# Kernel optimization log

Hardware: AMD Instinct MI355X
Metric: run time of the kernel (lower is better)

## Reference

```python
import jax, jax.numpy as jnp
import numpy as np

NUM_HEADS = 12


def setup_inputs() -> dict:
    key = jax.random.key(0)
    ks = jax.random.split(key, 4)
    N, L, C = 32, 577, 768  # L = 24*24 patches + 1 cls token
    x = jax.random.normal(ks[0], (N, L, C), dtype=jnp.float32)
    w_qkv = jax.random.normal(ks[1], (3 * C, C), dtype=jnp.float32) * 0.02
    w_proj = jax.random.normal(ks[2], (C, C), dtype=jnp.float32) * 0.02
    b_proj = jnp.zeros((C,), dtype=jnp.float32)
    w_dwc = jax.random.normal(ks[3], (C, 1, 3, 3), dtype=jnp.float32) * 0.02
    b_dwc = jnp.zeros((C,), dtype=jnp.float32)
    return {"x": x, "w_qkv": w_qkv, "w_proj": w_proj, "b_proj": b_proj,
            "w_dwc": w_dwc, "b_dwc": b_dwc}


def reference(x, w_qkv, w_proj, b_proj, w_dwc, b_dwc):
    N, L, C = x.shape
    H = NUM_HEADS
    hd = C // H
    h = w = int(L ** 0.5)  # 24; h*w == L-1 (cls token excluded)

    # qkv transform: (N, L, 3C) -> (3, N, H, L, hd)
    qkv = (x @ w_qkv.T).reshape(N, L, 3, H, hd).transpose(2, 0, 3, 1, 4)
    q, k, v = qkv[0], qkv[1], qkv[2]

    # graph-candidate attention (default: scaled dot-product softmax)
    scale = hd ** -0.5
    scores = jnp.einsum('bhqd,bhkd->bhqk', q, k) * scale
    attn = jax.nn.softmax(scores, axis=-1)
    out = jnp.einsum('bhqk,bhkd->bhqd', attn, v)  # (N, H, L, hd)
    out = out.transpose(0, 2, 1, 3).reshape(N, L, C)

    # depthwise conv on v (patch tokens only), NCHW layout
    v_ = v[:, :, 1:, :].transpose(0, 2, 1, 3).reshape(N, h, w, C).transpose(0, 3, 1, 2)
    dwc = jax.lax.conv_general_dilated(
        v_, w_dwc, window_strides=(1, 1), padding=((1, 1), (1, 1)),
        dimension_numbers=('NCHW', 'OIHW', 'NCHW'), feature_group_count=C)
    dwc = dwc + b_dwc[None, :, None, None]
    dwc = dwc.transpose(0, 2, 3, 1).reshape(N, L - 1, C)

    out = out.at[:, 1:, :].add(dwc)
    out = out @ w_proj.T + b_proj
    return out
```

## Files before the change

### kernel.cpp

```cpp
#include <hip/hip_runtime.h>

typedef short bf16x8 __attribute__((ext_vector_type(8)));
typedef float f32x4 __attribute__((ext_vector_type(4)));
typedef unsigned short u16;

#define NB 32
#define LSEQ 577
#define CD 768
#define NH 12
#define HD 64
#define MROWS (NB * LSEQ)
#define LPAD 584

#define GLD16(g, l)                                                    \
  __builtin_amdgcn_global_load_lds(                                    \
      (const __attribute__((address_space(1))) void*)(g),              \
      (__attribute__((address_space(3))) void*)(l), 16, 0, 0)

__device__ __forceinline__ u16 f2bf(float f) {
  union { float f; unsigned u; } v; v.f = f;
  unsigned u = v.u + 0x7fffu + ((v.u >> 16) & 1u);
  return (u16)(u >> 16);
}
__device__ __forceinline__ float bf2f(u16 s) {
  union { unsigned u; float f; } v; v.u = ((unsigned)s) << 16;
  return v.f;
}

__global__ __launch_bounds__(256) void cvt_bf16(
    const float* __restrict__ src, u16* __restrict__ dst, int n4) {
  int i = blockIdx.x * 256 + threadIdx.x;
  if (i < n4) {
    float4 v = reinterpret_cast<const float4*>(src)[i];
    ushort4 o;
    o.x = f2bf(v.x); o.y = f2bf(v.y); o.z = f2bf(v.z); o.w = f2bf(v.w);
    reinterpret_cast<ushort4*>(dst)[i] = o;
  }
}

__global__ __launch_bounds__(512, 2) void qkv_gemm(
    const u16* __restrict__ xb, const u16* __restrict__ wqb,
    u16* __restrict__ qb, u16* __restrict__ kb, u16* __restrict__ vtb) {
  __shared__ __align__(16) u16 As[3][256 * 32];
  __shared__ __align__(16) u16 Bs[3][256 * 32];
  const int m0 = blockIdx.x * 256;
  const int n0 = blockIdx.y * 256;
  const int t = threadIdx.x;
  const int lane = t & 63, wid = t >> 6;
  const int wm = wid >> 2, wn = wid & 3;
  const int g = lane >> 4, cl = lane & 15;

  const int r16 = lane >> 2;
  const int scol = (lane & 3) * 8;
  const int ra0 = wid * 16 + r16;
  const int ra1 = 128 + wid * 16 + r16;
  int gm0 = m0 + ra0; gm0 = gm0 < MROWS ? gm0 : MROWS - 1;
  int gm1 = m0 + ra1; gm1 = gm1 < MROWS ? gm1 : MROWS - 1;
  const u16* ax0 = xb + (size_t)gm0 * CD + scol;
  const u16* ax1 = xb + (size_t)gm1 * CD + scol;
  const u16* bx0 = wqb + (size_t)(n0 + ra0) * CD + scol;
  const u16* bx1 = wqb + (size_t)(n0 + ra1) * CD + scol;

  const f32x4 fz = {0.f, 0.f, 0.f, 0.f};
  f32x4 acc[8][4];
#pragma unroll
  for (int i = 0; i < 8; ++i)
#pragma unroll
    for (int j = 0; j < 4; ++j) acc[i][j] = fz;

#define QSTAGE(b, kt)                                  \
  do {                                                 \
    int kc = (kt) * 32;                                \
    GLD16(ax0 + kc, &As[b][wid * 512]);                \
    GLD16(ax1 + kc, &As[b][(wid + 8) * 512]);          \
    GLD16(bx0 + kc, &Bs[b][wid * 512]);                \
    GLD16(bx1 + kc, &Bs[b][(wid + 8) * 512]);          \
  } while (0)

  QSTAGE(0, 0);
  QSTAGE(1, 1);
  for (int kt = 0; kt < 24; ++kt) {
    const int cb = kt % 3;
    if (kt < 23) asm volatile("s_waitcnt vmcnt(4)" ::: "memory");
    else         asm volatile("s_waitcnt vmcnt(0)" ::: "memory");
    __builtin_amdgcn_s_barrier();
    if (kt < 22) QSTAGE((kt + 2) % 3, kt + 2);
    bf16x8 af[8], bfv[4];
#pragma unroll
    for (int mt = 0; mt < 8; ++mt)
      af[mt] = *reinterpret_cast<const bf16x8*>(&As[cb][(wm * 128 + mt * 16 + cl) * 32 + g * 8]);
#pragma unroll
    for (int nt = 0; nt < 4; ++nt)
      bfv[nt] = *reinterpret_cast<const bf16x8*>(&Bs[cb][(wn * 64 + nt * 16 + cl) * 32 + g * 8]);
    __builtin_amdgcn_s_setprio(1);
#pragma unroll
    for (int mt = 0; mt < 8; ++mt)
#pragma unroll
      for (int nt = 0; nt < 4; ++nt)
        acc[mt][nt] = __builtin_amdgcn_mfma_f32_16x16x32_bf16(af[mt], bfv[nt], acc[mt][nt], 0, 0, 0);
    __builtin_amdgcn_s_setprio(0);
  }
#undef QSTAGE

  const int which = n0 / CD;
  const int rem0 = n0 % CD;
#pragma unroll
  for (int mt = 0; mt < 8; ++mt) {
#pragma unroll
    for (int nt = 0; nt < 4; ++nt) {
      int rem = rem0 + wn * 64 + nt * 16 + cl;
      int hh = rem >> 6, d = rem & 63;
#pragma unroll
      for (int r = 0; r < 4; ++r) {
        int m = m0 + wm * 128 + mt * 16 + g * 4 + r;
        if (m < MROWS) {
          int nb = m / LSEQ, l = m - nb * LSEQ;
          if (which == 0)
            qb[(((size_t)nb * NH + hh) * LSEQ + l) * HD + d] = f2bf(acc[mt][nt][r] * 0.125f);
          else if (which == 1)
            kb[(((size_t)nb * NH + hh) * LSEQ + l) * HD + d] = f2bf(acc[mt][nt][r]);
          else
            vtb[(((size_t)nb * NH + hh) * HD + d) * LPAD + l] = f2bf(acc[mt][nt][r]);
        }
      }
    }
  }
}

__global__ __launch_bounds__(512) void attn_fwd(
    const u16* __restrict__ q, const u16* __restrict__ k,
    const u16* __restrict__ vt, u16* __restrict__ y) {
  __shared__ __align__(16) u16 Ks[64 * 72];
  __shared__ __align__(16) u16 Vts[64 * 72];
  __shared__ __align__(16) u16 Ps[8][16 * 72];

  const int qtile = blockIdx.x;
  const int h = blockIdx.y;
  const int nb = blockIdx.z;
  const int t = threadIdx.x;
  const int lane = t & 63, wid = t >> 6;
  const int g = lane >> 4, cl = lane & 15;

  const size_t hoff = ((size_t)nb * NH + h) * LSEQ * HD;
  const u16* qh = q + hoff;
  const u16* kh = k + hoff;
  const u16* vth = vt + ((size_t)nb * NH + h) * HD * LPAD;

  const int qbase = qtile * 128;
  const int qrow = qbase + wid * 16 + cl;
  const int qrc = qrow < LSEQ ? qrow : LSEQ - 1;
  bf16x8 qf0 = *reinterpret_cast<const bf16x8*>(qh + (size_t)qrc * HD + g * 8);
  bf16x8 qf1 = *reinterpret_cast<const bf16x8*>(qh + (size_t)qrc * HD + 32 + g * 8);

  const f32x4 fz = {0.f, 0.f, 0.f, 0.f};
  float mrow = -3.0e38f, lrow = 0.f;
  f32x4 oaccT[4];
#pragma unroll
  for (int dt = 0; dt < 4; ++dt) oaccT[dt] = fz;

  for (int kv = 0; kv < LSEQ; kv += 64) {
    {
      int row = t >> 3, c8 = (t & 7) << 3;
      int grow = kv + row;
      uint4 kd = {0, 0, 0, 0};
      if (grow < LSEQ) kd = *reinterpret_cast<const uint4*>(kh + (size_t)grow * HD + c8);
      *reinterpret_cast<uint4*>(&Ks[row * 72 + c8]) = kd;
      uint4 vd = *reinterpret_cast<const uint4*>(vth + (size_t)row * LPAD + kv + c8);
      *reinterpret_cast<uint4*>(&Vts[row * 72 + c8]) = vd;
    }
    __syncthreads();

    f32x4 sT[4];
#pragma unroll
    for (int nt = 0; nt < 4; ++nt) {
      bf16x8 a0 = *reinterpret_cast<const bf16x8*>(&Ks[(nt * 16 + cl) * 72 + g * 8]);
      bf16x8 a1 = *reinterpret_cast<const bf16x8*>(&Ks[(nt * 16 + cl) * 72 + 32 + g * 8]);
      f32x4 s = fz;
      s = __builtin_amdgcn_mfma_f32_16x16x32_bf16(a0, qf0, s, 0, 0, 0);
      s = __builtin_amdgcn_mfma_f32_16x16x32_bf16(a1, qf1, s, 0, 0, 0);
      sT[nt] = s;
    }

#pragma unroll
    for (int nt = 0; nt < 4; ++nt)
#pragma unroll
      for (int r = 0; r < 4; ++r)
        if (kv + nt * 16 + g * 4 + r >= LSEQ) sT[nt][r] = -3.0e38f;

    float pm = -3.0e38f;
#pragma unroll
    for (int nt = 0; nt < 4; ++nt)
#pragma unroll
      for (int r = 0; r < 4; ++r) pm = fmaxf(pm, sT[nt][r]);
    pm = fmaxf(pm, __shfl_xor(pm, 16));
    pm = fmaxf(pm, __shfl_xor(pm, 32));

    float nm = fmaxf(mrow, pm);
    float alpha = __expf(mrow - nm);
    mrow = nm;
    float ps = 0.f;
#pragma unroll
    for (int nt = 0; nt < 4; ++nt)
#pragma unroll
      for (int r = 0; r < 4; ++r) {
        float p = __expf(sT[nt][r] - nm);
        sT[nt][r] = p;
        ps += p;
      }
    ps += __shfl_xor(ps, 16);
    ps += __shfl_xor(ps, 32);
    lrow = lrow * alpha + ps;
#pragma unroll
    for (int dt = 0; dt < 4; ++dt) oaccT[dt] *= alpha;

#pragma unroll
    for (int nt = 0; nt < 4; ++nt) {
      ushort4 p4;
      p4.x = f2bf(sT[nt][0]); p4.y = f2bf(sT[nt][1]);
      p4.z = f2bf(sT[nt][2]); p4.w = f2bf(sT[nt][3]);
      *reinterpret_cast<ushort4*>(&Ps[wid][cl * 72 + nt * 16 + g * 4]) = p4;
    }
    __syncthreads();

#pragma unroll
    for (int kc = 0; kc < 2; ++kc) {
      bf16x8 pa = *reinterpret_cast<const bf16x8*>(&Ps[wid][cl * 72 + kc * 32 + g * 8]);
#pragma unroll
      for (int dt = 0; dt < 4; ++dt) {
        bf16x8 va = *reinterpret_cast<const bf16x8*>(&Vts[(dt * 16 + cl) * 72 + kc * 32 + g * 8]);
        oaccT[dt] = __builtin_amdgcn_mfma_f32_16x16x32_bf16(va, pa, oaccT[dt], 0, 0, 0);
      }
    }
    __syncthreads();
  }

  if (qrow < LSEQ) {
    float inv = 1.f / lrow;
#pragma unroll
    for (int dt = 0; dt < 4; ++dt) {
      ushort4 o4;
      o4.x = f2bf(oaccT[dt][0] * inv); o4.y = f2bf(oaccT[dt][1] * inv);
      o4.z = f2bf(oaccT[dt][2] * inv); o4.w = f2bf(oaccT[dt][3] * inv);
      *reinterpret_cast<ushort4*>(
          &y[((size_t)nb * LSEQ + qrow) * CD + h * HD + dt * 16 + g * 4]) = o4;
    }
  }
}

__global__ __launch_bounds__(256) void dwc_add(
    const u16* __restrict__ vt, const float* __restrict__ wd,
    const float* __restrict__ bd, u16* __restrict__ y) {
  __shared__ u16 V[32 * 588];
  const int d0 = blockIdx.x * 32;
  const int h = blockIdx.y;
  const int nb = blockIdx.z;
  const int t = threadIdx.x;
  const u16* vrow = vt + (((size_t)nb * NH + h) * HD + d0) * LPAD;

  for (int c = t; c < 32 * 73; c += 256) {
    int row = c / 73;
    int k0 = (c - row * 73) * 8;
    uint4 vv = *reinterpret_cast<const uint4*>(vrow + (size_t)row * LPAD + k0);
    const u16* vp = (const u16*)&vv;
    *reinterpret_cast<ushort4*>(&V[row * 588 + k0]) = *(const ushort4*)vp;
    *reinterpret_cast<ushort4*>(&V[row * 588 + k0 + 4]) = *(const ushort4*)(vp + 4);
  }
  __syncthreads();

  const int d = t & 31;
  const int c = h * HD + d0 + d;
  float w9[9];
#pragma unroll
  for (int j = 0; j < 9; ++j) w9[j] = wd[c * 9 + j];
  const float bias = bd[c];
  const u16* Vd = &V[d * 588];

  for (int it = 0; it < 72; ++it) {
    int li = (t >> 5) + it * 8;
    int py = li / 24, px = li - py * 24;
    float acc = bias;
#pragma unroll
    for (int ky = 0; ky < 3; ++ky) {
      int yy = py + ky - 1;
      if (yy < 0 || yy >= 24) continue;
      int base = 1 + yy * 24;
#pragma unroll
      for (int kx = 0; kx < 3; ++kx) {
        int xx = px + kx - 1;
        if (xx < 0 || xx >= 24) continue;
        acc += w9[ky * 3 + kx] * bf2f(Vd[base + xx]);
      }
    }
    size_t yi = ((size_t)nb * LSEQ + 1 + li) * CD + c;
    y[yi] = f2bf(bf2f(y[yi]) + acc);
  }
}

__global__ __launch_bounds__(256) void proj_gemm(
    const u16* __restrict__ yb, const u16* __restrict__ wpb,
    const float* __restrict__ bias, float* __restrict__ out) {
  __shared__ __align__(16) u16 As[2][128 * 32];
  __shared__ __align__(16) u16 Bs[2][128 * 32];
  const int m0 = blockIdx.x * 128;
  const int n0 = blockIdx.y * 128;
  const int t = threadIdx.x;
  const int lane = t & 63, wid = t >> 6;
  const int wm = wid >> 1, wn = wid & 1;
  const int g = lane >> 4, cl = lane & 15;

  const int srow = wid * 32 + (lane >> 2);
  const int scol = (lane & 3) * 8;
  int ga0 = m0 + srow;      ga0 = ga0 < MROWS ? ga0 : MROWS - 1;
  int ga1 = m0 + srow + 16; ga1 = ga1 < MROWS ? ga1 : MROWS - 1;
  const u16* asrc0 = yb + (size_t)ga0 * CD + scol;
  const u16* asrc1 = yb + (size_t)ga1 * CD + scol;
  const u16* bsrc0 = wpb + (size_t)(n0 + srow) * CD + scol;
  const u16* bsrc1 = wpb + (size_t)(n0 + srow + 16) * CD + scol;

  const f32x4 fz = {0.f, 0.f, 0.f, 0.f};
  f32x4 acc[4][4];
#pragma unroll
  for (int i = 0; i < 4; ++i)
#pragma unroll
    for (int j = 0; j < 4; ++j) acc[i][j] = fz;

#define PSTAGE(b, kt)                                   \
  do {                                                  \
    int kc = (kt) * 32;                                 \
    GLD16(asrc0 + kc, &As[b][wid * 1024]);              \
    GLD16(asrc1 + kc, &As[b][wid * 1024 + 512]);        \
    GLD16(bsrc0 + kc, &Bs[b][wid * 1024]);              \
    GLD16(bsrc1 + kc, &Bs[b][wid * 1024 + 512]);        \
  } while (0)

  PSTAGE(0, 0);
  __syncthreads();
  int cur = 0;
  for (int kt = 0; kt < 24; ++kt) {
    if (kt < 23) PSTAGE(cur ^ 1, kt + 1);
    bf16x8 af[4], bfv[4];
#pragma unroll
    for (int mt = 0; mt < 4; ++mt)
      af[mt] = *reinterpret_cast<const bf16x8*>(&As[cur][(wm * 64 + mt * 16 + cl) * 32 + g * 8]);
#pragma unroll
    for (int nt = 0; nt < 4; ++nt)
      bfv[nt] = *reinterpret_cast<const bf16x8*>(&Bs[cur][(wn * 64 + nt * 16 + cl) * 32 + g * 8]);
    __builtin_amdgcn_s_setprio(1);
#pragma unroll
    for (int mt = 0; mt < 4; ++mt)
#pragma unroll
      for (int nt = 0; nt < 4; ++nt)
        acc[mt][nt] = __builtin_amdgcn_mfma_f32_16x16x32_bf16(af[mt], bfv[nt], acc[mt][nt], 0, 0, 0);
    __builtin_amdgcn_s_setprio(0);
    __syncthreads();
    cur ^= 1;
  }
#undef PSTAGE

#pragma unroll
  for (int nt = 0; nt < 4; ++nt) {
    int n = n0 + wn * 64 + nt * 16 + cl;
    float bn = bias[n];
#pragma unroll
    for (int mt = 0; mt < 4; ++mt)
#pragma unroll
      for (int r = 0; r < 4; ++r) {
        int m = m0 + wm * 64 + mt * 16 + g * 4 + r;
        if (m < MROWS) out[(size_t)m * CD + n] = acc[mt][nt][r] + bn;
      }
  }
}

extern "C" void kernel_launch(void* const* d_in, const int* in_sizes, int n_in,
                              void* d_out, int out_size, void* d_ws, size_t ws_size,
                              hipStream_t stream) {
  const float* x = (const float*)d_in[0];
  const float* w_qkv = (const float*)d_in[1];
  const float* w_proj = (const float*)d_in[2];
  const float* b_proj = (const float*)d_in[3];
  const float* w_dwc = (const float*)d_in[4];
  const float* b_dwc = (const float*)d_in[5];
  float* out = (float*)d_out;

  const size_t SEG = (size_t)NB * NH * LSEQ * HD;
  const size_t SEGT = (size_t)NB * NH * HD * LPAD;
  const size_t YN = (size_t)MROWS * CD;
  u16* yb = (u16*)d_ws;
  u16* xb = yb;
  u16* qb = yb + YN;
  u16* kb = qb + SEG;
  u16* vtb = kb + SEG;
  u16* wqb = vtb + SEGT;
  u16* wpb = wqb + (size_t)3 * CD * CD;

  cvt_bf16<<<dim3((int)(YN / 4 / 256)), 256, 0, stream>>>(x, xb, (int)(YN / 4));
  cvt_bf16<<<dim3(3 * CD * CD / 4 / 256), 256, 0, stream>>>(w_qkv, wqb, 3 * CD * CD / 4);
  cvt_bf16<<<dim3(CD * CD / 4 / 256), 256, 0, stream>>>(w_proj, wpb, CD * CD / 4);
  qkv_gemm<<<dim3(73, 9), 512, 0, stream>>>(xb, wqb, qb, kb, vtb);
  attn_fwd<<<dim3(5, 12, 32), 512, 0, stream>>>(qb, kb, vtb, yb);
  dwc_add<<<dim3(2, 12, 32), 256, 0, stream>>>(vtb, w_dwc, b_dwc, yb);
  proj_gemm<<<dim3(145, 6), 256, 0, stream>>>(yb, wpb, b_proj, out);
}
```

Baseline: 394.4 us.

## Remap GEMM blocks per XCD, double-buffer attention K/V, inline-asm LDS reads

Both GEMMs now use a 1D grid whose block ids are remapped so each XCD processes a contiguous range of output tiles, aiming for better L2 reuse of A/B panels. The QKV GEMM loads its fragments from LDS with explicit ds_read_b128 asm, followed by a full lgkmcnt wait and a sched barrier. The attention kernel double-buffers K/V tiles in LDS: the next tile is prefetched into registers during compute and stored afterwards, which removes one syncthreads per iteration and adds setprio around the MFMAs. The costs are more LDS use in attention and fixed schedules that the compiler can no longer reorder.

```diff
diff --git a/kernel.cpp b/kernel.cpp
--- a/kernel.cpp
+++ b/kernel.cpp
@@ -3,6 +3,7 @@
 typedef short bf16x8 __attribute__((ext_vector_type(8)));
 typedef float f32x4 __attribute__((ext_vector_type(4)));
 typedef unsigned short u16;
+typedef __attribute__((address_space(3))) const u16* lds_cptr;
 
 #define NB 32
 #define LSEQ 577
@@ -16,6 +17,10 @@
   __builtin_amdgcn_global_load_lds(                                    \
       (const __attribute__((address_space(1))) void*)(g),              \
       (__attribute__((address_space(3))) void*)(l), 16, 0, 0)
+
+#define DSR(dst, base, ofs)                                            \
+  asm volatile("ds_read_b128 %0, %1 offset:" #ofs                      \
+               : "=v"(dst) : "v"((lds_cptr)(base)))
 
 __device__ __forceinline__ u16 f2bf(float f) {
   union { float f; unsigned u; } v; v.f = f;
@@ -43,8 +48,11 @@
     u16* __restrict__ qb, u16* __restrict__ kb, u16* __restrict__ vtb) {
   __shared__ __align__(16) u16 As[3][256 * 32];
   __shared__ __align__(16) u16 Bs[3][256 * 32];
-  const int m0 = blockIdx.x * 256;
-  const int n0 = blockIdx.y * 256;
+  const int id = blockIdx.x;
+  const int xcd = id & 7, pos = id >> 3;
+  const int wg = (xcd == 0 ? pos : 83 + (xcd - 1) * 82 + pos);
+  const int m0 = (wg / 9) * 256;
+  const int n0 = (wg % 9) * 256;
   const int t = threadIdx.x;
   const int lane = t & 63, wid = t >> 6;
   const int wm = wid >> 2, wn = wid & 3;
@@ -81,17 +89,21 @@
   QSTAGE(1, 1);
   for (int kt = 0; kt < 24; ++kt) {
     const int cb = kt % 3;
-    if (kt < 23) asm volatile("s_waitcnt vmcnt(4)" ::: "memory");
-    else         asm volatile("s_waitcnt vmcnt(0)" ::: "memory");
+    if (kt < 23) asm volatile("s_waitcnt vmcnt(4)");
+    else         asm volatile("s_waitcnt vmcnt(0)");
     __builtin_amdgcn_s_barrier();
     if (kt < 22) QSTAGE((kt + 2) % 3, kt + 2);
+    const u16* pa = &As[cb][(wm * 128 + cl) * 32 + g * 8];
+    const u16* pb = &Bs[cb][(wn * 64 + cl) * 32 + g * 8];
     bf16x8 af[8], bfv[4];
-#pragma unroll
-    for (int mt = 0; mt < 8; ++mt)
-      af[mt] = *reinterpret_cast<const bf16x8*>(&As[cb][(wm * 128 + mt * 16 + cl) * 32 + g * 8]);
-#pragma unroll
-    for (int nt = 0; nt < 4; ++nt)
-      bfv[nt] = *reinterpret_cast<const bf16x8*>(&Bs[cb][(wn * 64 + nt * 16 + cl) * 32 + g * 8]);
+    DSR(af[0], pa, 0);    DSR(af[1], pa, 1024);
+    DSR(af[2], pa, 2048); DSR(af[3], pa, 3072);
+    DSR(af[4], pa, 4096); DSR(af[5], pa, 5120);
+    DSR(af[6], pa, 6144); DSR(af[7], pa, 7168);
+    DSR(bfv[0], pb, 0);    DSR(bfv[1], pb, 1024);
+    DSR(bfv[2], pb, 2048); DSR(bfv[3], pb, 3072);
+    asm volatile("s_waitcnt lgkmcnt(0)");
+    __builtin_amdgcn_sched_barrier(0);
     __builtin_amdgcn_s_setprio(1);
 #pragma unroll
     for (int mt = 0; mt < 8; ++mt)
@@ -130,15 +142,15 @@
 __global__ __launch_bounds__(512) void attn_fwd(
     const u16* __restrict__ q, const u16* __restrict__ k,
     const u16* __restrict__ vt, u16* __restrict__ y) {
-  __shared__ __align__(16) u16 Ks[64 * 72];
-  __shared__ __align__(16) u16 Vts[64 * 72];
+  __shared__ __align__(16) u16 Ks[2][64 * 72];
+  __shared__ __align__(16) u16 Vts[2][64 * 72];
   __shared__ __align__(16) u16 Ps[8][16 * 72];
 
   const int qtile = blockIdx.x;
   const int h = blockIdx.y;
   const int nb = blockIdx.z;
-  const int t = threadIdx.x;
-  const int lane = t & 63, wid = t >> 6;
+  const int tid = threadIdx.x;
+  const int lane = tid & 63, wid = tid >> 6;
   const int g = lane >> 4, cl = lane & 15;
 
   const size_t hoff = ((size_t)nb * NH + h) * LSEQ * HD;
@@ -158,28 +170,42 @@
 #pragma unroll
   for (int dt = 0; dt < 4; ++dt) oaccT[dt] = fz;
 
-  for (int kv = 0; kv < LSEQ; kv += 64) {
-    {
-      int row = t >> 3, c8 = (t & 7) << 3;
-      int grow = kv + row;
-      uint4 kd = {0, 0, 0, 0};
-      if (grow < LSEQ) kd = *reinterpret_cast<const uint4*>(kh + (size_t)grow * HD + c8);
-      *reinterpret_cast<uint4*>(&Ks[row * 72 + c8]) = kd;
-      uint4 vd = *reinterpret_cast<const uint4*>(vth + (size_t)row * LPAD + kv + c8);
-      *reinterpret_cast<uint4*>(&Vts[row * 72 + c8]) = vd;
-    }
-    __syncthreads();
+  const int srow = tid >> 3, sc8 = (tid & 7) << 3;
+  const u16* kptr = kh + (size_t)srow * HD + sc8;
+  const u16* vptr = vth + (size_t)srow * LPAD + sc8;
+
+  {
+    uint4 kd = *reinterpret_cast<const uint4*>(kptr);
+    uint4 vd = *reinterpret_cast<const uint4*>(vptr);
+    *reinterpret_cast<uint4*>(&Ks[0][srow * 72 + sc8]) = kd;
+    *reinterpret_cast<uint4*>(&Vts[0][srow * 72 + sc8]) = vd;
+  }
+  __syncthreads();
+
+  const int NT = 10;
+  for (int tt = 0; tt < NT; ++tt) {
+    const int c = tt & 1;
+    const int kv = tt * 64;
+    uint4 kn = {0, 0, 0, 0}, vn = {0, 0, 0, 0};
+    const bool pre = (tt + 1 < NT);
+    if (pre) {
+      int grow = kv + 64 + srow;
+      if (grow < LSEQ) kn = *reinterpret_cast<const uint4*>(kptr + (size_t)(kv + 64) * HD);
+      vn = *reinterpret_cast<const uint4*>(vptr + (kv + 64));
+    }
 
     f32x4 sT[4];
+    __builtin_amdgcn_s_setprio(1);
 #pragma unroll
     for (int nt = 0; nt < 4; ++nt) {
-      bf16x8 a0 = *reinterpret_cast<const bf16x8*>(&Ks[(nt * 16 + cl) * 72 + g * 8]);
-      bf16x8 a1 = *reinterpret_cast<const bf16x8*>(&Ks[(nt * 16 + cl) * 72 + 32 + g * 8]);
+      bf16x8 a0 = *reinterpret_cast<const bf16x8*>(&Ks[c][(nt * 16 + cl) * 72 + g * 8]);
+      bf16x8 a1 = *reinterpret_cast<const bf16x8*>(&Ks[c][(nt * 16 + cl) * 72 + 32 + g * 8]);
       f32x4 s = fz;
       s = __builtin_amdgcn_mfma_f32_16x16x32_bf16(a0, qf0, s, 0, 0, 0);
       s = __builtin_amdgcn_mfma_f32_16x16x32_bf16(a1, qf1, s, 0, 0, 0);
       sT[nt] = s;
     }
+    __builtin_amdgcn_s_setprio(0);
 
 #pragma unroll
     for (int nt = 0; nt < 4; ++nt)
@@ -220,16 +246,22 @@
       p4.z = f2bf(sT[nt][2]); p4.w = f2bf(sT[nt][3]);
       *reinterpret_cast<ushort4*>(&Ps[wid][cl * 72 + nt * 16 + g * 4]) = p4;
     }
-    __syncthreads();
-
+
+    __builtin_amdgcn_s_setprio(1);
 #pragma unroll
     for (int kc = 0; kc < 2; ++kc) {
       bf16x8 pa = *reinterpret_cast<const bf16x8*>(&Ps[wid][cl * 72 + kc * 32 + g * 8]);
 #pragma unroll
       for (int dt = 0; dt < 4; ++dt) {
-        bf16x8 va = *reinterpret_cast<const bf16x8*>(&Vts[(dt * 16 + cl) * 72 + kc * 32 + g * 8]);
+        bf16x8 va = *reinterpret_cast<const bf16x8*>(&Vts[c][(dt * 16 + cl) * 72 + kc * 32 + g * 8]);
         oaccT[dt] = __builtin_amdgcn_mfma_f32_16x16x32_bf16(va, pa, oaccT[dt], 0, 0, 0);
       }
+    }
+    __builtin_amdgcn_s_setprio(0);
+
+    if (pre) {
+      *reinterpret_cast<uint4*>(&Ks[c ^ 1][srow * 72 + sc8]) = kn;
+      *reinterpret_cast<uint4*>(&Vts[c ^ 1][srow * 72 + sc8]) = vn;
     }
     __syncthreads();
   }
@@ -301,8 +333,11 @@
     const float* __restrict__ bias, float* __restrict__ out) {
   __shared__ __align__(16) u16 As[2][128 * 32];
   __shared__ __align__(16) u16 Bs[2][128 * 32];
-  const int m0 = blockIdx.x * 128;
-  const int n0 = blockIdx.y * 128;
+  const int id = blockIdx.x;
+  const int xcd = id & 7, pos = id >> 3;
+  const int wg = (xcd < 6 ? xcd * 109 + pos : 654 + (xcd - 6) * 108 + pos);
+  const int m0 = (wg / 6) * 128;
+  const int n0 = (wg % 6) * 128;
   const int t = threadIdx.x;
   const int lane = t & 63, wid = t >> 6;
   const int wm = wid >> 1, wn = wid & 1;
@@ -396,8 +431,8 @@
   cvt_bf16<<<dim3((int)(YN / 4 / 256)), 256, 0, stream>>>(x, xb, (int)(YN / 4));
   cvt_bf16<<<dim3(3 * CD * CD / 4 / 256), 256, 0, stream>>>(w_qkv, wqb, 3 * CD * CD / 4);
   cvt_bf16<<<dim3(CD * CD / 4 / 256), 256, 0, stream>>>(w_proj, wpb, CD * CD / 4);
-  qkv_gemm<<<dim3(73, 9), 512, 0, stream>>>(xb, wqb, qb, kb, vtb);
+  qkv_gemm<<<dim3(657), 512, 0, stream>>>(xb, wqb, qb, kb, vtb);
   attn_fwd<<<dim3(5, 12, 32), 512, 0, stream>>>(qb, kb, vtb, yb);
   dwc_add<<<dim3(2, 12, 32), 256, 0, stream>>>(vtb, w_dwc, b_dwc, yb);
-  proj_gemm<<<dim3(145, 6), 256, 0, stream>>>(yb, wpb, b_proj, out);
-}
+  proj_gemm<<<dim3(870), 256, 0, stream>>>(yb, wpb, b_proj, out);
+}
```

After: 354.5 us. 1.11x faster.
